# Performance work log

Hardware: AMD Instinct MI355X
Metric: run time of the kernel (lower is better)

Reference implementation:

```python
import jax, jax.numpy as jnp
import numpy as np

N_NODES = 100000
N_EDGES = 1600000
IN_CH = 64
HID = 64
OUT_CH = 1


def setup_inputs() -> dict:
    key = jax.random.key(0)
    ks = jax.random.split(key, 6)
    x = jax.random.normal(ks[0], (N_NODES, IN_CH), dtype=jnp.float32)
    edge_index = jax.random.randint(ks[1], (2, N_EDGES), 0, N_NODES, dtype=jnp.int64)
    edge_weight = jax.random.uniform(ks[2], (N_EDGES,), dtype=jnp.float32)
    W1 = jax.random.normal(ks[3], (IN_CH, HID), dtype=jnp.float32) / np.sqrt(IN_CH)
    b1 = jnp.zeros((HID,), dtype=jnp.float32)
    W2 = jax.random.normal(ks[4], (HID, OUT_CH), dtype=jnp.float32) / np.sqrt(HID)
    b2 = jnp.zeros((OUT_CH,), dtype=jnp.float32)
    return {"x": x, "edge_index": edge_index, "edge_weight": edge_weight,
            "W1": W1, "b1": b1, "W2": W2, "b2": b2}


def _gcn_conv(x, row, col, ew, W, b, n_nodes):
    # PyG GCNConv: add self-loops (weight 1), symmetric deg normalization,
    # linear (no bias) -> message x_j * norm -> sum at target -> + bias.
    loop = jnp.arange(n_nodes, dtype=row.dtype)
    r = jnp.concatenate([row, loop])
    c = jnp.concatenate([col, loop])
    w = jnp.concatenate([ew, jnp.ones((n_nodes,), dtype=ew.dtype)])
    deg = jax.ops.segment_sum(w, c, num_segments=n_nodes)  # [N]
    dinv = jnp.where(deg > 0, jax.lax.rsqrt(deg), 0.0)
    norm = dinv[r] * w * dinv[c]  # [E+N]
    h = x @ W  # [N, out]
    msg = h[r] * norm[:, None]  # [E+N, out] gather
    out = jax.ops.segment_sum(msg, c, num_segments=n_nodes)  # scatter-add
    return out + b


def reference(x, edge_index, edge_weight, W1, b1, W2, b2):
    row, col = edge_index[0], edge_index[1]
    n = x.shape[0]
    h = _gcn_conv(x, row, col, edge_weight, W1, b1, n)
    h = jax.nn.relu(h)
    out = _gcn_conv(h, row, col, edge_weight, W2, b2, n)
    return out
```

## Files before the change

### kernel.cpp

```cpp
#include <hip/hip_runtime.h>


#define N_NODES 100000
#define N_EDGES 1600000
#define CNT_SHIFT 42
#define SUM_MASK ((1ull << CNT_SHIFT) - 1)
#define NBUCK 1563
#define NB1 512
#define EPB 3125

typedef _Float16 half2v __attribute__((ext_vector_type(2)));

__global__ void p1_hist(const int* __restrict__ idx, int* __restrict__ hist) {
    __shared__ int h[NBUCK];
    int t = threadIdx.x, blk = blockIdx.x;
    for (int i = t; i < NBUCK; i += 256) h[i] = 0;
    __syncthreads();
    int e0 = blk * EPB;
    for (int i = t; i < EPB; i += 256) {
        int c = idx[N_EDGES + e0 + i];
        atomicAdd(&h[c >> 6], 1);
    }
    __syncthreads();
    for (int i = t; i < NBUCK; i += 256) hist[(size_t)i * NB1 + blk] = h[i];
}

__global__ void p2a_scan(int* __restrict__ hist, int* __restrict__ btot) {
    __shared__ int s[NB1];
    int t = threadIdx.x, b = blockIdx.x;
    int v = hist[(size_t)b * NB1 + t];
    s[t] = v;
    __syncthreads();
#pragma unroll
    for (int d = 1; d < NB1; d <<= 1) {
        int u = (t >= d) ? s[t - d] : 0;
        __syncthreads();
        s[t] += u;
        __syncthreads();
    }
    hist[(size_t)b * NB1 + t] = s[t] - v;
    if (t == NB1 - 1) btot[b] = s[NB1 - 1];
}

__global__ void p2b_scan(const int* __restrict__ btot, int* __restrict__ boff) {
    __shared__ int s[256];
    __shared__ int carry;
    int t = threadIdx.x;
    if (t == 0) carry = 0;
    __syncthreads();
    for (int base = 0; base < NBUCK; base += 256) {
        int i = base + t;
        int v = (i < NBUCK) ? btot[i] : 0;
        s[t] = v;
        __syncthreads();
#pragma unroll
        for (int d = 1; d < 256; d <<= 1) {
            int u = (t >= d) ? s[t - d] : 0;
            __syncthreads();
            s[t] += u;
            __syncthreads();
        }
        if (i < NBUCK) boff[i] = carry + s[t] - v;
        __syncthreads();
        if (t == 255) carry += s[255];
        __syncthreads();
    }
    if (t == 0) boff[NBUCK] = carry;
}

__global__ void p3_part(const int* __restrict__ idx, const float* __restrict__ w,
                        const int* __restrict__ hist, const int* __restrict__ boff,
                        float2* __restrict__ bin) {
    __shared__ int h[NBUCK];
    int t = threadIdx.x, blk = blockIdx.x;
    for (int i = t; i < NBUCK; i += 256) h[i] = 0;
    __syncthreads();
    int e0 = blk * EPB;
    for (int i = t; i < EPB; i += 256) {
        int e = e0 + i;
        int r = idx[e];
        int c = idx[N_EDGES + e];
        int b = c >> 6;
        int lr = atomicAdd(&h[b], 1);
        int pos = boff[b] + hist[(size_t)b * NB1 + blk] + lr;
        bin[pos] = make_float2(__int_as_float(r | ((c & 63) << 20)), w[e]);
    }
}

__global__ void p4a_count(const float2* __restrict__ bin, const int* __restrict__ boff,
                          int* __restrict__ cnt, int* __restrict__ off,
                          float* __restrict__ dinv) {
    __shared__ unsigned long long pk[64];
    int t = threadIdx.x, b = blockIdx.x;
    if (t < 64) pk[t] = 0ull;
    __syncthreads();
    int s0 = boff[b], s1 = boff[b + 1];
    for (int j = s0 + t; j < s1; j += 256) {
        float2 p = bin[j];
        int cl = (__float_as_int(p.x) >> 20) & 63;
        unsigned long long add =
            (1ull << CNT_SHIFT) | (unsigned long long)(p.y * 4294967296.0f);
        atomicAdd(&pk[cl], add);
    }
    __syncthreads();
    if (t < 64) {
        unsigned long long p = pk[t];
        int c = (int)(p >> CNT_SHIFT);
        int x = c;
#pragma unroll
        for (int d = 1; d < 64; d <<= 1) {
            int u = __shfl_up(x, d, 64);
            if (t >= d) x += u;
        }
        int node = b * 64 + t;
        if (node < N_NODES) {
            off[node] = s0 + x - c;
            cnt[node] = c;
            float deg = 1.0f + (float)(p & SUM_MASK) * 2.3283064365386963e-10f;
            dinv[node] = rsqrtf(deg);
        }
    }
}

__global__ void p4b_place(const float2* __restrict__ bin, const int* __restrict__ boff,
                          const int* __restrict__ off, const float* __restrict__ dinv,
                          float2* __restrict__ pairs) {
    __shared__ int rk[64];
    int t = threadIdx.x, b = blockIdx.x;
    if (t < 64) rk[t] = 0;
    __syncthreads();
    int s0 = boff[b], s1 = boff[b + 1];
    for (int j = s0 + t; j < s1; j += 256) {
        float2 p = bin[j];
        int bits = __float_as_int(p.x);
        int r = bits & 0xFFFFF;
        int cl = (bits >> 20) & 63;
        int c = (b << 6) + cl;
        int rank = atomicAdd(&rk[cl], 1);
        float norm = dinv[r] * p.y * dinv[c];
        pairs[off[c] + rank] = make_float2(__int_as_float(r), norm);
    }
}

__global__ void gemm1(const float* __restrict__ x, const float* __restrict__ W1,
                      _Float16* __restrict__ h1) {
    __shared__ float w1s[64 * 64];
    __shared__ float xs[16 * 64];
    int t = threadIdx.x;
    int row0 = blockIdx.x * 16;

    const float4* W4 = (const float4*)W1;
    float4* w1s4 = (float4*)w1s;
#pragma unroll
    for (int i = 0; i < 4; i++) w1s4[t + 256 * i] = W4[t + 256 * i];
    ((float4*)xs)[t] = ((const float4*)(x + (size_t)row0 * 64))[t];
    __syncthreads();

    int col = t & 63;
    int r0 = t >> 6;
    float acc0 = 0.f, acc1 = 0.f, acc2 = 0.f, acc3 = 0.f;
#pragma unroll
    for (int k = 0; k < 64; k++) {
        float wv = w1s[k * 64 + col];
        acc0 += xs[(r0     ) * 64 + k] * wv;
        acc1 += xs[(r0 +  4) * 64 + k] * wv;
        acc2 += xs[(r0 +  8) * 64 + k] * wv;
        acc3 += xs[(r0 + 12) * 64 + k] * wv;
    }
    float accs[4] = {acc0, acc1, acc2, acc3};
#pragma unroll
    for (int j = 0; j < 4; j++)
        h1[(row0 + r0 + 4 * j) * 64 + col] = (_Float16)accs[j];
}

__global__ void gather1(const half2v* __restrict__ h1v, const float2* __restrict__ pairs,
                        const int* __restrict__ off, const int* __restrict__ cnt,
                        const float* __restrict__ dinv, const float* __restrict__ b1,
                        const float* __restrict__ W2, const float* __restrict__ b2,
                        float* __restrict__ h2, float* __restrict__ out, int n) {
    int t = threadIdx.x;
    int lane = t & 63;
    int half = lane >> 5;
    int cl = lane & 31;
    int dst = blockIdx.x * 4 + (t >> 6);
    if (dst >= n) return;
    int beg = off[dst];
    int end = beg + cnt[dst];
    float di = dinv[dst];
    float a0 = 0.f, a1 = 0.f, b0 = 0.f, b1a = 0.f;
    float c0 = 0.f, c1 = 0.f, d0 = 0.f, d1 = 0.f;
    int j = beg + half;
    for (; j + 6 < end; j += 8) {
        float2 p0 = pairs[j], p1 = pairs[j + 2], p2 = pairs[j + 4], p3 = pairs[j + 6];
        half2v v0 = h1v[__float_as_int(p0.x) * 32 + cl];
        half2v v1 = h1v[__float_as_int(p1.x) * 32 + cl];
        half2v v2 = h1v[__float_as_int(p2.x) * 32 + cl];
        half2v v3 = h1v[__float_as_int(p3.x) * 32 + cl];
        a0 += p0.y * (float)v0[0]; a1 += p0.y * (float)v0[1];
        b0 += p1.y * (float)v1[0]; b1a += p1.y * (float)v1[1];
        c0 += p2.y * (float)v2[0]; c1 += p2.y * (float)v2[1];
        d0 += p3.y * (float)v3[0]; d1 += p3.y * (float)v3[1];
    }
    for (; j < end; j += 2) {
        float2 p = pairs[j];
        half2v v = h1v[__float_as_int(p.x) * 32 + cl];
        a0 += p.y * (float)v[0]; a1 += p.y * (float)v[1];
    }
    float t0 = (a0 + b0) + (c0 + d0);
    float t1 = (a1 + b1a) + (c1 + d1);
    t0 += __shfl_xor(t0, 32, 64);
    t1 += __shfl_xor(t1, 32, 64);
    half2v sv = h1v[dst * 32 + cl];
    t0 += (float)sv[0] * di * di;
    t1 += (float)sv[1] * di * di;
    float2 b1p = ((const float2*)b1)[cl];
    float v0 = fmaxf(t0 + b1p.x, 0.0f);
    float v1 = fmaxf(t1 + b1p.y, 0.0f);
    float2 w2p = ((const float2*)W2)[cl];
    float p = v0 * w2p.x + v1 * w2p.y;
#pragma unroll
    for (int o = 16; o > 0; o >>= 1) p += __shfl_xor(p, o, 64);
    if (lane == 0) {
        h2[dst] = p;
        out[dst] = b2[0] + p * di * di;
    }
}

__global__ void gather2(const float2* __restrict__ pairs, const int* __restrict__ off,
                        const int* __restrict__ cnt, const float* __restrict__ h2,
                        float* __restrict__ out, int n) {
    int i = blockIdx.x * blockDim.x + threadIdx.x;
    if (i >= n) return;
    int beg = off[i];
    int end = beg + cnt[i];
    float s = 0.f;
#pragma unroll 4
    for (int j = beg; j < end; j++) {
        float2 p = pairs[j];
        s += p.y * h2[__float_as_int(p.x)];
    }
    out[i] += s;
}

extern "C" void kernel_launch(void* const* d_in, const int* in_sizes, int n_in,
                              void* d_out, int out_size, void* d_ws, size_t ws_size,
                              hipStream_t stream) {
    const float* x   = (const float*)d_in[0];
    const int*   idx = (const int*)d_in[1];
    const float* ew  = (const float*)d_in[2];
    const float* W1  = (const float*)d_in[3];
    const float* b1  = (const float*)d_in[4];
    const float* W2  = (const float*)d_in[5];
    const float* b2  = (const float*)d_in[6];
    float* out = (float*)d_out;

    const int N = N_NODES;
    const int E = N_EDGES;

    float* ws = (float*)d_ws;
    int*    off  = (int*)ws;
    int*    cnt  = (int*)(ws + (size_t)N);
    float*  dinv = ws + 2 * (size_t)N;
    int*    boff = (int*)(ws + 3 * (size_t)N);
    int*    btot = (int*)(ws + 3 * (size_t)N + 1564);
    int*    hist = (int*)(ws + 303128);
    float2* bin  = (float2*)(ws + 303128 + 800256);
    _Float16* h1 = (_Float16*)(ws + 303128);
    float2* pairs = (float2*)(ws + 303128 + 6400000);
    float*  h2   = ws + 303128 + 6400000 + 3200000;

    p1_hist<<<NB1, 256, 0, stream>>>(idx, hist);
    p2a_scan<<<NBUCK, NB1, 0, stream>>>(hist, btot);
    p2b_scan<<<1, 256, 0, stream>>>(btot, boff);
    p3_part<<<NB1, 256, 0, stream>>>(idx, ew, hist, boff, bin);
    p4a_count<<<NBUCK, 256, 0, stream>>>(bin, boff, cnt, off, dinv);
    p4b_place<<<NBUCK, 256, 0, stream>>>(bin, boff, off, dinv, pairs);
    gemm1<<<N / 16, 256, 0, stream>>>(x, W1, h1);
    gather1<<<(N + 3) / 4, 256, 0, stream>>>((const half2v*)h1, pairs, off, cnt, dinv,
                                             b1, W2, b2, h2, out, N);
    gather2<<<(N + 255) / 256, 256, 0, stream>>>(pairs, off, cnt, h2, out, N);
}
```

Baseline: 262.8 us.

## Widen CSR buckets to 256 nodes, retile gemm1, deepen gather1 unroll

Buckets now cover 256 destination nodes instead of 64, which cuts the bucket count and the size of the histogram and scan. The partition kernel caches per-bucket base offsets in shared memory, and the count and place kernels run 512 threads per bucket with a shared-memory scan. gemm1 computes 64 rows per block with float4 register tiles and packed half stores. gather1 uses 128-thread blocks and a 16-edge unrolled inner loop. Row indices now get only 17 bits, which still covers 100000 nodes, but the larger buckets raise shared-memory atomic contention per block.

```diff
diff --git a/kernel.cpp b/kernel.cpp
--- a/kernel.cpp
+++ b/kernel.cpp
@@ -5,7 +5,8 @@
 #define N_EDGES 1600000
 #define CNT_SHIFT 42
 #define SUM_MASK ((1ull << CNT_SHIFT) - 1)
-#define NBUCK 1563
+#define BSZ 256
+#define NBUCK 391
 #define NB1 512
 #define EPB 3125
 
@@ -19,7 +20,7 @@
     int e0 = blk * EPB;
     for (int i = t; i < EPB; i += 256) {
         int c = idx[N_EDGES + e0 + i];
-        atomicAdd(&h[c >> 6], 1);
+        atomicAdd(&h[c >> 8], 1);
     }
     __syncthreads();
     for (int i = t; i < NBUCK; i += 256) hist[(size_t)i * NB1 + blk] = h[i];
@@ -43,78 +44,80 @@
 }
 
 __global__ void p2b_scan(const int* __restrict__ btot, int* __restrict__ boff) {
-    __shared__ int s[256];
-    __shared__ int carry;
+    __shared__ int s[512];
     int t = threadIdx.x;
-    if (t == 0) carry = 0;
-    __syncthreads();
-    for (int base = 0; base < NBUCK; base += 256) {
-        int i = base + t;
-        int v = (i < NBUCK) ? btot[i] : 0;
-        s[t] = v;
-        __syncthreads();
-#pragma unroll
-        for (int d = 1; d < 256; d <<= 1) {
-            int u = (t >= d) ? s[t - d] : 0;
-            __syncthreads();
-            s[t] += u;
-            __syncthreads();
-        }
-        if (i < NBUCK) boff[i] = carry + s[t] - v;
-        __syncthreads();
-        if (t == 255) carry += s[255];
-        __syncthreads();
-    }
-    if (t == 0) boff[NBUCK] = carry;
+    int v = (t < NBUCK) ? btot[t] : 0;
+    s[t] = v;
+    __syncthreads();
+#pragma unroll
+    for (int d = 1; d < 512; d <<= 1) {
+        int u = (t >= d) ? s[t - d] : 0;
+        __syncthreads();
+        s[t] += u;
+        __syncthreads();
+    }
+    if (t < NBUCK) boff[t] = s[t] - v;
+    if (t == 511) boff[NBUCK] = s[511];
 }
 
 __global__ void p3_part(const int* __restrict__ idx, const float* __restrict__ w,
                         const int* __restrict__ hist, const int* __restrict__ boff,
                         float2* __restrict__ bin) {
     __shared__ int h[NBUCK];
+    __shared__ int base[NBUCK];
     int t = threadIdx.x, blk = blockIdx.x;
-    for (int i = t; i < NBUCK; i += 256) h[i] = 0;
+    for (int i = t; i < NBUCK; i += 256) {
+        h[i] = 0;
+        base[i] = boff[i] + hist[(size_t)i * NB1 + blk];
+    }
     __syncthreads();
     int e0 = blk * EPB;
     for (int i = t; i < EPB; i += 256) {
         int e = e0 + i;
         int r = idx[e];
         int c = idx[N_EDGES + e];
-        int b = c >> 6;
+        int b = c >> 8;
         int lr = atomicAdd(&h[b], 1);
-        int pos = boff[b] + hist[(size_t)b * NB1 + blk] + lr;
-        bin[pos] = make_float2(__int_as_float(r | ((c & 63) << 20)), w[e]);
+        bin[base[b] + lr] = make_float2(__int_as_float(r | ((c & 255) << 17)), w[e]);
     }
 }
 
 __global__ void p4a_count(const float2* __restrict__ bin, const int* __restrict__ boff,
                           int* __restrict__ cnt, int* __restrict__ off,
                           float* __restrict__ dinv) {
-    __shared__ unsigned long long pk[64];
+    __shared__ unsigned long long pk[BSZ];
+    __shared__ int s[BSZ];
     int t = threadIdx.x, b = blockIdx.x;
-    if (t < 64) pk[t] = 0ull;
+    if (t < BSZ) pk[t] = 0ull;
     __syncthreads();
     int s0 = boff[b], s1 = boff[b + 1];
-    for (int j = s0 + t; j < s1; j += 256) {
+    for (int j = s0 + t; j < s1; j += 512) {
         float2 p = bin[j];
-        int cl = (__float_as_int(p.x) >> 20) & 63;
+        int cl = (__float_as_int(p.x) >> 17) & 255;
         unsigned long long add =
             (1ull << CNT_SHIFT) | (unsigned long long)(p.y * 4294967296.0f);
         atomicAdd(&pk[cl], add);
     }
     __syncthreads();
-    if (t < 64) {
-        unsigned long long p = pk[t];
-        int c = (int)(p >> CNT_SHIFT);
-        int x = c;
-#pragma unroll
-        for (int d = 1; d < 64; d <<= 1) {
-            int u = __shfl_up(x, d, 64);
-            if (t >= d) x += u;
-        }
-        int node = b * 64 + t;
+    unsigned long long p = 0;
+    int c = 0;
+    if (t < BSZ) {
+        p = pk[t];
+        c = (int)(p >> CNT_SHIFT);
+        s[t] = c;
+    }
+    __syncthreads();
+#pragma unroll
+    for (int d = 1; d < BSZ; d <<= 1) {
+        int u = (t >= d && t < BSZ) ? s[t - d] : 0;
+        __syncthreads();
+        if (t < BSZ) s[t] += u;
+        __syncthreads();
+    }
+    if (t < BSZ) {
+        int node = b * BSZ + t;
         if (node < N_NODES) {
-            off[node] = s0 + x - c;
+            off[node] = s0 + s[t] - c;
             cnt[node] = c;
             float deg = 1.0f + (float)(p & SUM_MASK) * 2.3283064365386963e-10f;
             dinv[node] = rsqrtf(deg);
@@ -125,17 +128,17 @@
 __global__ void p4b_place(const float2* __restrict__ bin, const int* __restrict__ boff,
                           const int* __restrict__ off, const float* __restrict__ dinv,
                           float2* __restrict__ pairs) {
-    __shared__ int rk[64];
+    __shared__ int rk[BSZ];
     int t = threadIdx.x, b = blockIdx.x;
-    if (t < 64) rk[t] = 0;
+    if (t < BSZ) rk[t] = 0;
     __syncthreads();
     int s0 = boff[b], s1 = boff[b + 1];
-    for (int j = s0 + t; j < s1; j += 256) {
+    for (int j = s0 + t; j < s1; j += 512) {
         float2 p = bin[j];
         int bits = __float_as_int(p.x);
-        int r = bits & 0xFFFFF;
-        int cl = (bits >> 20) & 63;
-        int c = (b << 6) + cl;
+        int r = bits & 0x1FFFF;
+        int cl = (bits >> 17) & 255;
+        int c = (b << 8) + cl;
         int rank = atomicAdd(&rk[cl], 1);
         float norm = dinv[r] * p.y * dinv[c];
         pairs[off[c] + rank] = make_float2(__int_as_float(r), norm);
@@ -145,32 +148,50 @@
 __global__ void gemm1(const float* __restrict__ x, const float* __restrict__ W1,
                       _Float16* __restrict__ h1) {
     __shared__ float w1s[64 * 64];
-    __shared__ float xs[16 * 64];
+    __shared__ float xs[64 * 64];
     int t = threadIdx.x;
-    int row0 = blockIdx.x * 16;
+    int row0 = blockIdx.x * 64;
 
     const float4* W4 = (const float4*)W1;
     float4* w1s4 = (float4*)w1s;
-#pragma unroll
-    for (int i = 0; i < 4; i++) w1s4[t + 256 * i] = W4[t + 256 * i];
-    ((float4*)xs)[t] = ((const float4*)(x + (size_t)row0 * 64))[t];
-    __syncthreads();
-
-    int col = t & 63;
-    int r0 = t >> 6;
-    float acc0 = 0.f, acc1 = 0.f, acc2 = 0.f, acc3 = 0.f;
-#pragma unroll
+    float4* xs4 = (float4*)xs;
+    const float4* X4 = (const float4*)(x + (size_t)row0 * 64);
+#pragma unroll
+    for (int i = 0; i < 4; i++) {
+        w1s4[t + 256 * i] = W4[t + 256 * i];
+        int gr = row0 + ((t + 256 * i) >> 4);
+        xs4[t + 256 * i] = (gr < N_NODES) ? X4[t + 256 * i]
+                                          : make_float4(0.f, 0.f, 0.f, 0.f);
+    }
+    __syncthreads();
+
+    int cq = t & 15;
+    int rq = t >> 4;
+    float4 acc0 = {0,0,0,0}, acc1 = {0,0,0,0}, acc2 = {0,0,0,0}, acc3 = {0,0,0,0};
+#pragma unroll 4
     for (int k = 0; k < 64; k++) {
-        float wv = w1s[k * 64 + col];
-        acc0 += xs[(r0     ) * 64 + k] * wv;
-        acc1 += xs[(r0 +  4) * 64 + k] * wv;
-        acc2 += xs[(r0 +  8) * 64 + k] * wv;
-        acc3 += xs[(r0 + 12) * 64 + k] * wv;
-    }
-    float accs[4] = {acc0, acc1, acc2, acc3};
-#pragma unroll
-    for (int j = 0; j < 4; j++)
-        h1[(row0 + r0 + 4 * j) * 64 + col] = (_Float16)accs[j];
+        float4 wv = w1s4[k * 16 + cq];
+        float x0 = xs[(rq     ) * 64 + k];
+        float x1 = xs[(rq + 16) * 64 + k];
+        float x2 = xs[(rq + 32) * 64 + k];
+        float x3 = xs[(rq + 48) * 64 + k];
+        acc0.x += x0*wv.x; acc0.y += x0*wv.y; acc0.z += x0*wv.z; acc0.w += x0*wv.w;
+        acc1.x += x1*wv.x; acc1.y += x1*wv.y; acc1.z += x1*wv.z; acc1.w += x1*wv.w;
+        acc2.x += x2*wv.x; acc2.y += x2*wv.y; acc2.z += x2*wv.z; acc2.w += x2*wv.w;
+        acc3.x += x3*wv.x; acc3.y += x3*wv.y; acc3.z += x3*wv.z; acc3.w += x3*wv.w;
+    }
+    float4 accs[4] = {acc0, acc1, acc2, acc3};
+#pragma unroll
+    for (int i = 0; i < 4; i++) {
+        int row = row0 + rq + 16 * i;
+        if (row < N_NODES) {
+            half2v h01 = {(_Float16)accs[i].x, (_Float16)accs[i].y};
+            half2v h23 = {(_Float16)accs[i].z, (_Float16)accs[i].w};
+            half2v* dst = (half2v*)(h1 + (size_t)row * 64 + 4 * cq);
+            dst[0] = h01;
+            dst[1] = h23;
+        }
+    }
 }
 
 __global__ void gather1(const half2v* __restrict__ h1v, const float2* __restrict__ pairs,
@@ -182,7 +203,7 @@
     int lane = t & 63;
     int half = lane >> 5;
     int cl = lane & 31;
-    int dst = blockIdx.x * 4 + (t >> 6);
+    int dst = blockIdx.x * 2 + (t >> 6);
     if (dst >= n) return;
     int beg = off[dst];
     int end = beg + cnt[dst];
@@ -190,6 +211,26 @@
     float a0 = 0.f, a1 = 0.f, b0 = 0.f, b1a = 0.f;
     float c0 = 0.f, c1 = 0.f, d0 = 0.f, d1 = 0.f;
     int j = beg + half;
+    for (; j + 14 < end; j += 16) {
+        float2 p0 = pairs[j],      p1 = pairs[j + 2],  p2 = pairs[j + 4],  p3 = pairs[j + 6];
+        float2 p4 = pairs[j + 8],  p5 = pairs[j + 10], p6 = pairs[j + 12], p7 = pairs[j + 14];
+        half2v v0 = h1v[__float_as_int(p0.x) * 32 + cl];
+        half2v v1 = h1v[__float_as_int(p1.x) * 32 + cl];
+        half2v v2 = h1v[__float_as_int(p2.x) * 32 + cl];
+        half2v v3 = h1v[__float_as_int(p3.x) * 32 + cl];
+        half2v v4 = h1v[__float_as_int(p4.x) * 32 + cl];
+        half2v v5 = h1v[__float_as_int(p5.x) * 32 + cl];
+        half2v v6 = h1v[__float_as_int(p6.x) * 32 + cl];
+        half2v v7 = h1v[__float_as_int(p7.x) * 32 + cl];
+        a0 += p0.y * (float)v0[0]; a1 += p0.y * (float)v0[1];
+        b0 += p1.y * (float)v1[0]; b1a += p1.y * (float)v1[1];
+        c0 += p2.y * (float)v2[0]; c1 += p2.y * (float)v2[1];
+        d0 += p3.y * (float)v3[0]; d1 += p3.y * (float)v3[1];
+        a0 += p4.y * (float)v4[0]; a1 += p4.y * (float)v4[1];
+        b0 += p5.y * (float)v5[0]; b1a += p5.y * (float)v5[1];
+        c0 += p6.y * (float)v6[0]; c1 += p6.y * (float)v6[1];
+        d0 += p7.y * (float)v7[0]; d1 += p7.y * (float)v7[1];
+    }
     for (; j + 6 < end; j += 8) {
         float2 p0 = pairs[j], p1 = pairs[j + 2], p2 = pairs[j + 4], p3 = pairs[j + 6];
         half2v v0 = h1v[__float_as_int(p0.x) * 32 + cl];
@@ -262,21 +303,21 @@
     int*    cnt  = (int*)(ws + (size_t)N);
     float*  dinv = ws + 2 * (size_t)N;
     int*    boff = (int*)(ws + 3 * (size_t)N);
-    int*    btot = (int*)(ws + 3 * (size_t)N + 1564);
-    int*    hist = (int*)(ws + 303128);
-    float2* bin  = (float2*)(ws + 303128 + 800256);
-    _Float16* h1 = (_Float16*)(ws + 303128);
-    float2* pairs = (float2*)(ws + 303128 + 6400000);
-    float*  h2   = ws + 303128 + 6400000 + 3200000;
+    int*    btot = (int*)(ws + 3 * (size_t)N + 392);
+    int*    hist = (int*)(ws + 300784);
+    float2* bin  = (float2*)(ws + 300784 + 200192);
+    _Float16* h1 = (_Float16*)(ws + 300784);
+    float2* pairs = (float2*)(ws + 3700976);
+    float*  h2   = ws + 6900976;
 
     p1_hist<<<NB1, 256, 0, stream>>>(idx, hist);
     p2a_scan<<<NBUCK, NB1, 0, stream>>>(hist, btot);
-    p2b_scan<<<1, 256, 0, stream>>>(btot, boff);
+    p2b_scan<<<1, 512, 0, stream>>>(btot, boff);
     p3_part<<<NB1, 256, 0, stream>>>(idx, ew, hist, boff, bin);
-    p4a_count<<<NBUCK, 256, 0, stream>>>(bin, boff, cnt, off, dinv);
-    p4b_place<<<NBUCK, 256, 0, stream>>>(bin, boff, off, dinv, pairs);
-    gemm1<<<N / 16, 256, 0, stream>>>(x, W1, h1);
-    gather1<<<(N + 3) / 4, 256, 0, stream>>>((const half2v*)h1, pairs, off, cnt, dinv,
+    p4a_count<<<NBUCK, 512, 0, stream>>>(bin, boff, cnt, off, dinv);
+    p4b_place<<<NBUCK, 512, 0, stream>>>(bin, boff, off, dinv, pairs);
+    gemm1<<<(N + 63) / 64, 256, 0, stream>>>(x, W1, h1);
+    gather1<<<(N + 1) / 2, 128, 0, stream>>>((const half2v*)h1, pairs, off, cnt, dinv,
                                              b1, W2, b2, h2, out, N);
     gather2<<<(N + 255) / 256, 256, 0, stream>>>(pairs, off, cnt, h2, out, N);
 }
```

After: 228.4 us. 1.15x faster.
